# Kernel tuning notes

Hardware: AMD Instinct MI355X
Metric: run time of the kernel (lower is better)

Reference implementation:

```python
import jax, jax.numpy as jnp
import numpy as np

N_EMBED = 1024
HEAD_SIZE = 64
BLOCK_SIZE = 2048

def setup_inputs() -> dict:
    key = jax.random.key(0)
    kx, kq, kk, kv = jax.random.split(key, 4)
    scale = N_EMBED ** -0.5
    x = jax.random.normal(kx, (8, 2048, N_EMBED), dtype=jnp.float32)
    # nn.Linear weights stored as [out, in]; we keep [in, out] for x @ W
    Wq = jax.random.normal(kq, (N_EMBED, HEAD_SIZE), dtype=jnp.float32) * scale
    Wk = jax.random.normal(kk, (N_EMBED, HEAD_SIZE), dtype=jnp.float32) * scale
    Wv = jax.random.normal(kv, (N_EMBED, HEAD_SIZE), dtype=jnp.float32) * scale
    return {"x": x, "Wq": Wq, "Wk": Wk, "Wv": Wv}

def reference(x, Wq, Wk, Wv):
    B, T, C = x.shape
    q = x @ Wq  # [B,T,H]
    k = x @ Wk
    v = x @ Wv
    # NOTE: original scales by C**-0.5 (n_embed), not head_size**-0.5
    wei = jnp.einsum('bth,bsh->bts', q, k) * (C ** -0.5)  # [B,T,T]
    causal = jnp.tril(jnp.ones((T, T), dtype=bool))
    wei = jnp.where(causal, wei, -jnp.inf)
    wei = jax.nn.softmax(wei, axis=-1)
    out = jnp.einsum('bts,bsh->bth', wei, v)  # [B,T,H]
    return out
```

## Files before the change

kernel.cpp:

```cpp
#include <hip/hip_runtime.h>

#define B_ 8
#define T_ 2048
#define C_ 1024
#define H_ 64

typedef __attribute__((ext_vector_type(8))) short short8;
typedef __attribute__((ext_vector_type(4))) float floatx4;
typedef __attribute__((ext_vector_type(4))) int intx4;

static __device__ __forceinline__ unsigned short f2bf(float f) {
  unsigned int u = __builtin_bit_cast(unsigned int, f);
  u += 0x7FFFu + ((u >> 16) & 1u);
  return (unsigned short)(u >> 16);
}
static __device__ __forceinline__ unsigned short f2bf_t(float f) {
  return (unsigned short)(__builtin_bit_cast(unsigned int, f) >> 16);
}
static __device__ __forceinline__ float bf2f(unsigned short u) {
  return __builtin_bit_cast(float, ((unsigned int)u) << 16);
}
static __device__ __forceinline__ unsigned int fbits(float f) {
  return __builtin_bit_cast(unsigned int, f);
}

typedef const __attribute__((address_space(1))) unsigned int* gp1_t;
typedef __attribute__((address_space(3))) unsigned int* lp3_t;
static __device__ __forceinline__ void gl_lds16(const void* g, void* l) {
  __builtin_amdgcn_global_load_lds((gp1_t)g, (lp3_t)l, 16, 0, 0);
}

__global__ __launch_bounds__(256) void conv_w(const float* __restrict__ wq,
    const float* __restrict__ wk, const float* __restrict__ wv,
    unsigned short* __restrict__ wf) {
  int c = blockIdx.x * 256 + threadIdx.x;
  int lane = c & 63;
  int t = c >> 6;
  int ng = t % 12;
  int kk = t / 12;
  int k0 = kk * 32 + (lane >> 4) * 8;
  int n = ng * 16 + (lane & 15);
  const float* src;
  int col;
  float scale = 1.0f;
  if (n < 64)       { src = wq; col = n;       scale = 0.03125f * 1.44269504088896340736f; }
  else if (n < 128) { src = wk; col = n - 64;  }
  else              { src = wv; col = n - 128; }
  unsigned short o[8];
#pragma unroll
  for (int j = 0; j < 8; ++j) o[j] = f2bf(src[(size_t)(k0 + j) * H_ + col] * scale);
  *(uint4*)&wf[(size_t)c * 8] = *(const uint4*)o;
}

__global__ __launch_bounds__(256) void qkv_proj(
    const float* __restrict__ x, const unsigned short* __restrict__ wf,
    unsigned short* __restrict__ qo, unsigned short* __restrict__ kf,
    unsigned short* __restrict__ vf) {
  __shared__ float XL[2][2048];
  int tid = threadIdx.x;
  int wave = tid >> 6, lane = tid & 63;
  int lane4 = lane & 15, quad = lane >> 4;
  int m0 = blockIdx.x * 32;

  floatx4 acc[2][3];
#pragma unroll
  for (int mt = 0; mt < 2; ++mt)
#pragma unroll
    for (int nt = 0; nt < 3; ++nt) acc[mt][nt] = (floatx4)0.0f;

#pragma unroll
  for (int j = 0; j < 2; ++j) {
    int p = (wave * 2 + j) * 64 + lane;
    int r = p >> 4, pc = p & 15;
    int cl = (pc & 8) | ((pc ^ (r & 7)) & 7);
    gl_lds16(&x[(size_t)(m0 + r) * C_ + cl * 4], &XL[0][(wave * 2 + j) * 256]);
  }
  __syncthreads();

  for (int kt = 0; kt < 16; ++kt) {
    int buf = kt & 1;
    if (kt < 15) {
      int k0 = (kt + 1) * 64;
#pragma unroll
      for (int j = 0; j < 2; ++j) {
        int p = (wave * 2 + j) * 64 + lane;
        int r = p >> 4, pc = p & 15;
        int cl = (pc & 8) | ((pc ^ (r & 7)) & 7);
        gl_lds16(&x[(size_t)(m0 + r) * C_ + k0 + cl * 4], &XL[buf ^ 1][(wave * 2 + j) * 256]);
      }
    }

#pragma unroll
    for (int ks = 0; ks < 2; ++ks) {
      short8 b[3];
#pragma unroll
      for (int nt = 0; nt < 3; ++nt)
        b[nt] = *(const short8*)&wf[(size_t)(((kt * 2 + ks) * 12) + wave * 3 + nt) * 512 + lane * 8];
      short8 a[2];
#pragma unroll
      for (int mt = 0; mt < 2; ++mt) {
        int r = mt * 16 + lane4;
        int cl0 = ks * 8 + quad * 2;
        int pc0 = (cl0 & 8) | ((cl0 ^ (r & 7)) & 7);
        int pc1 = ((cl0 + 1) & 8) | (((cl0 + 1) ^ (r & 7)) & 7);
        float4 f0 = *(const float4*)&XL[buf][r * 64 + pc0 * 4];
        float4 f1 = *(const float4*)&XL[buf][r * 64 + pc1 * 4];
        intx4 pk;
        pk[0] = (int)__builtin_amdgcn_perm(fbits(f0.y), fbits(f0.x), 0x07060302u);
        pk[1] = (int)__builtin_amdgcn_perm(fbits(f0.w), fbits(f0.z), 0x07060302u);
        pk[2] = (int)__builtin_amdgcn_perm(fbits(f1.y), fbits(f1.x), 0x07060302u);
        pk[3] = (int)__builtin_amdgcn_perm(fbits(f1.w), fbits(f1.z), 0x07060302u);
        a[mt] = __builtin_bit_cast(short8, pk);
      }
#pragma unroll
      for (int mt = 0; mt < 2; ++mt)
#pragma unroll
        for (int nt = 0; nt < 3; ++nt)
          acc[mt][nt] = __builtin_amdgcn_mfma_f32_16x16x32_bf16(a[mt], b[nt], acc[mt][nt], 0, 0, 0);
    }
    __syncthreads();
  }

  unsigned short* VTB = (unsigned short*)&XL[0][0];
  unsigned short* KB  = VTB + 5120;
#pragma unroll
  for (int mt = 0; mt < 2; ++mt)
#pragma unroll
    for (int nt = 0; nt < 3; ++nt) {
      int n = wave * 48 + nt * 16 + lane4;
#pragma unroll
      for (int rr = 0; rr < 4; ++rr) {
        unsigned short val = f2bf(acc[mt][nt][rr]);
        int lrow = mt * 16 + quad * 4 + rr;
        if (n < 64)       qo[(size_t)(m0 + lrow) * H_ + n] = val;
        else if (n < 128) KB[lrow * 72 + (n - 64)] = val;
        else              VTB[(n - 128) * 40 + lrow] = val;
      }
    }
  __syncthreads();
  {
    int bb = m0 >> 11, t0 = m0 & 2047;
    int st = t0 >> 6, off = t0 & 63;
    int ks = tid >> 7, ctl = (tid >> 6) & 1, ln = tid & 63;
    int ct = (off >> 4) + ctl;
    int tl = ctl * 16 + (ln & 15);
    int h0 = ks * 32 + (ln >> 4) * 8;
    uint4 kd = *(const uint4*)&KB[tl * 72 + h0];
    *(uint4*)&kf[((size_t)((bb * 32 + st) * 2 + ks) * 4 + ct) * 512 + ln * 8] = kd;
    int nt = tid >> 6, l4 = tid & 15, qs = (tid >> 4) & 3;
    int ksv = off >> 5;
    uint4 vd = *(const uint4*)&VTB[(nt * 16 + l4) * 40 + qs * 8];
    *(uint4*)&vf[((size_t)((bb * 32 + st) * 2 + ksv) * 4 + nt) * 512 + (tid & 63) * 8] = vd;
  }
}

__global__ __launch_bounds__(256) void attn(
    const unsigned short* __restrict__ qi, const unsigned short* __restrict__ Kf,
    const unsigned short* __restrict__ Vf, unsigned short* __restrict__ Op,
    float* __restrict__ lsum) {
  __shared__ unsigned short PL[4][16][72];

  int tid = threadIdx.x;
  int wave = tid >> 6, lane = tid & 63;
  int lane4 = lane & 15, quad = lane >> 4;
  int qt = 31 - (int)blockIdx.x;
  int b = blockIdx.y, split = blockIdx.z;
  int qb = qt * 64;
  int base = b * T_;

  int ntile = qt + 1;
  int sBeg = (split * ntile) >> 2;
  int sEnd = ((split + 1) * ntile) >> 2;

  short8 aq[2];
#pragma unroll
  for (int ks = 0; ks < 2; ++ks)
    aq[ks] = *(const short8*)&qi[(size_t)(base + qb + wave * 16 + lane4) * H_ + ks * 32 + quad * 8];

  float lrow[4];
  floatx4 o[4];
#pragma unroll
  for (int r = 0; r < 4; ++r) lrow[r] = 0.0f;
#pragma unroll
  for (int nt = 0; nt < 4; ++nt) o[nt] = (floatx4)0.0f;

  for (int st = sBeg; st < sEnd; ++st) {
    size_t tb = (size_t)(b * 32 + st) * 8;
    short8 bk[2][4], bv[2][4];
#pragma unroll
    for (int ks = 0; ks < 2; ++ks)
#pragma unroll
      for (int ct = 0; ct < 4; ++ct)
        bk[ks][ct] = *(const short8*)&Kf[(tb + ks * 4 + ct) * 512 + lane * 8];
#pragma unroll
    for (int ks = 0; ks < 2; ++ks)
#pragma unroll
      for (int nt = 0; nt < 4; ++nt)
        bv[ks][nt] = *(const short8*)&Vf[(tb + ks * 4 + nt) * 512 + lane * 8];

    floatx4 sacc[4];
#pragma unroll
    for (int ct = 0; ct < 4; ++ct) sacc[ct] = (floatx4)0.0f;
#pragma unroll
    for (int ks = 0; ks < 2; ++ks)
#pragma unroll
      for (int ct = 0; ct < 4; ++ct)
        sacc[ct] = __builtin_amdgcn_mfma_f32_16x16x32_bf16(aq[ks], bk[ks][ct], sacc[ct], 0, 0, 0);

    if (st == qt) {
#pragma unroll
      for (int ct = 0; ct < 4; ++ct)
#pragma unroll
        for (int r = 0; r < 4; ++r) {
          int qrow = wave * 16 + quad * 4 + r;
          int scol = ct * 16 + lane4;
          if (scol > qrow) sacc[ct][r] = -3.0e38f;
        }
    }

#pragma unroll
    for (int ct = 0; ct < 4; ++ct)
#pragma unroll
      for (int r = 0; r < 4; ++r) {
        float p = exp2f(sacc[ct][r] - 8.0f);
        lrow[r] += p;
        PL[wave][quad * 4 + r][ct * 16 + lane4] = f2bf_t(p);
      }

#pragma unroll
    for (int ks = 0; ks < 2; ++ks) {
      short8 pa = *(const short8*)&PL[wave][lane4][ks * 32 + quad * 8];
#pragma unroll
      for (int nt = 0; nt < 4; ++nt)
        o[nt] = __builtin_amdgcn_mfma_f32_16x16x32_bf16(pa, bv[ks][nt], o[nt], 0, 0, 0);
    }
  }

#pragma unroll
  for (int off = 1; off < 16; off <<= 1)
#pragma unroll
    for (int r = 0; r < 4; ++r) lrow[r] += __shfl_xor(lrow[r], off);

  size_t pbase = (((size_t)split * 8 + b) * 32 + qt) * 64;
#pragma unroll
  for (int r = 0; r < 4; ++r) {
    int row = wave * 16 + quad * 4 + r;
#pragma unroll
    for (int nt = 0; nt < 4; ++nt)
      Op[(pbase + row) * 64 + nt * 16 + lane4] = f2bf(o[nt][r]);
    if (lane4 == 0) lsum[pbase + row] = lrow[r];
  }
}

__global__ __launch_bounds__(256) void merge_splits(
    const unsigned short* __restrict__ Op, const float* __restrict__ lsum,
    float* __restrict__ out) {
  int idx = blockIdx.x * 256 + threadIdx.x;
  int row = idx >> 4;
  int h4 = (idx & 15) * 4;
  int b = row >> 11, t = row & 2047;
  int qt = t >> 6, r = t & 63;
  float O0 = 0.f, O1 = 0.f, O2 = 0.f, O3 = 0.f, l = 0.f;
#pragma unroll
  for (int s = 0; s < 4; ++s) {
    size_t p = (((size_t)s * 8 + b) * 32 + qt) * 64 + r;
    l += lsum[p];
    ushort4 ov = *(const ushort4*)&Op[p * 64 + h4];
    O0 += bf2f(ov.x); O1 += bf2f(ov.y); O2 += bf2f(ov.z); O3 += bf2f(ov.w);
  }
  float inv = 1.0f / l;
  float4 res = make_float4(O0 * inv, O1 * inv, O2 * inv, O3 * inv);
  *(float4*)&out[(size_t)row * H_ + h4] = res;
}

extern "C" void kernel_launch(void* const* d_in, const int* in_sizes, int n_in,
                              void* d_out, int out_size, void* d_ws, size_t ws_size,
                              hipStream_t stream) {
  const float* x  = (const float*)d_in[0];
  const float* wq = (const float*)d_in[1];
  const float* wk = (const float*)d_in[2];
  const float* wv = (const float*)d_in[3];
  float* out = (float*)d_out;

  char* ws = (char*)d_ws;
  unsigned short* wf = (unsigned short*)ws;
  unsigned short* qb = (unsigned short*)(ws + 393216);
  unsigned short* kf = (unsigned short*)(ws + 2490368);
  unsigned short* vf = (unsigned short*)(ws + 4587520);
  unsigned short* Op = (unsigned short*)(ws + 6684672);
  float*          ls = (float*)(ws + 15073280);

  conv_w<<<96, 256, 0, stream>>>(wq, wk, wv, wf);
  qkv_proj<<<512, 256, 0, stream>>>(x, wf, qb, kf, vf);
  attn<<<dim3(32, 8, 4), 256, 0, stream>>>(qb, kf, vf, Op, ls);
  merge_splits<<<1024, 256, 0, stream>>>(Op, ls, out);
}
```

Baseline: 137.4 us.

## Halve QKV projection row tile and load whole x tile into LDS upfront

The projection kernel now handles 16 rows per block instead of 32 and launches 1024 blocks. The full 16x1024 fp32 slice of x (64KB) is loaded into LDS in one go, which replaces the double-buffered 64-column pipeline and removes the per-iteration barriers. The launch bounds request two blocks per CU. The aim is more parallelism and fewer syncs, at the cost of less reuse of the weight fragments (each B load now feeds one MFMA row tile instead of two) and no overlap between loading x and computing. The K/V scatter epilogue is rewritten for the 16-row tile.

Result: slower. 141.6 us (+3.1%).

```diff
diff --git a/kernel.cpp b/kernel.cpp
--- a/kernel.cpp
+++ b/kernel.cpp
@@ -52,105 +52,90 @@
   *(uint4*)&wf[(size_t)c * 8] = *(const uint4*)o;
 }
 
-__global__ __launch_bounds__(256) void qkv_proj(
+__global__ __launch_bounds__(256, 2) void qkv_proj(
     const float* __restrict__ x, const unsigned short* __restrict__ wf,
     unsigned short* __restrict__ qo, unsigned short* __restrict__ kf,
     unsigned short* __restrict__ vf) {
-  __shared__ float XL[2][2048];
+  __shared__ float XL[16384];
   int tid = threadIdx.x;
   int wave = tid >> 6, lane = tid & 63;
   int lane4 = lane & 15, quad = lane >> 4;
-  int m0 = blockIdx.x * 32;
-
-  floatx4 acc[2][3];
-#pragma unroll
-  for (int mt = 0; mt < 2; ++mt)
-#pragma unroll
-    for (int nt = 0; nt < 3; ++nt) acc[mt][nt] = (floatx4)0.0f;
-
-#pragma unroll
-  for (int j = 0; j < 2; ++j) {
-    int p = (wave * 2 + j) * 64 + lane;
-    int r = p >> 4, pc = p & 15;
-    int cl = (pc & 8) | ((pc ^ (r & 7)) & 7);
-    gl_lds16(&x[(size_t)(m0 + r) * C_ + cl * 4], &XL[0][(wave * 2 + j) * 256]);
+  int m0 = blockIdx.x * 16;
+
+#pragma unroll
+  for (int j = 0; j < 16; ++j) {
+    int p = (wave * 16 + j) * 64 + lane;
+    int r = p >> 8, pc = p & 255;
+    int cl = (pc & ~7) | ((pc ^ (r & 7)) & 7);
+    gl_lds16(&x[(size_t)(m0 + r) * C_ + cl * 4], &XL[(wave * 16 + j) * 256]);
   }
   __syncthreads();
 
+  floatx4 acc[3];
+#pragma unroll
+  for (int nt = 0; nt < 3; ++nt) acc[nt] = (floatx4)0.0f;
+
+#pragma unroll 4
   for (int kt = 0; kt < 16; ++kt) {
-    int buf = kt & 1;
-    if (kt < 15) {
-      int k0 = (kt + 1) * 64;
-#pragma unroll
-      for (int j = 0; j < 2; ++j) {
-        int p = (wave * 2 + j) * 64 + lane;
-        int r = p >> 4, pc = p & 15;
-        int cl = (pc & 8) | ((pc ^ (r & 7)) & 7);
-        gl_lds16(&x[(size_t)(m0 + r) * C_ + k0 + cl * 4], &XL[buf ^ 1][(wave * 2 + j) * 256]);
-      }
-    }
-
 #pragma unroll
     for (int ks = 0; ks < 2; ++ks) {
       short8 b[3];
 #pragma unroll
       for (int nt = 0; nt < 3; ++nt)
         b[nt] = *(const short8*)&wf[(size_t)(((kt * 2 + ks) * 12) + wave * 3 + nt) * 512 + lane * 8];
-      short8 a[2];
-#pragma unroll
-      for (int mt = 0; mt < 2; ++mt) {
-        int r = mt * 16 + lane4;
-        int cl0 = ks * 8 + quad * 2;
-        int pc0 = (cl0 & 8) | ((cl0 ^ (r & 7)) & 7);
-        int pc1 = ((cl0 + 1) & 8) | (((cl0 + 1) ^ (r & 7)) & 7);
-        float4 f0 = *(const float4*)&XL[buf][r * 64 + pc0 * 4];
-        float4 f1 = *(const float4*)&XL[buf][r * 64 + pc1 * 4];
-        intx4 pk;
-        pk[0] = (int)__builtin_amdgcn_perm(fbits(f0.y), fbits(f0.x), 0x07060302u);
-        pk[1] = (int)__builtin_amdgcn_perm(fbits(f0.w), fbits(f0.z), 0x07060302u);
-        pk[2] = (int)__builtin_amdgcn_perm(fbits(f1.y), fbits(f1.x), 0x07060302u);
-        pk[3] = (int)__builtin_amdgcn_perm(fbits(f1.w), fbits(f1.z), 0x07060302u);
-        a[mt] = __builtin_bit_cast(short8, pk);
-      }
-#pragma unroll
-      for (int mt = 0; mt < 2; ++mt)
-#pragma unroll
-        for (int nt = 0; nt < 3; ++nt)
-          acc[mt][nt] = __builtin_amdgcn_mfma_f32_16x16x32_bf16(a[mt], b[nt], acc[mt][nt], 0, 0, 0);
-    }
-    __syncthreads();
-  }
-
-  unsigned short* VTB = (unsigned short*)&XL[0][0];
-  unsigned short* KB  = VTB + 5120;
-#pragma unroll
-  for (int mt = 0; mt < 2; ++mt)
-#pragma unroll
-    for (int nt = 0; nt < 3; ++nt) {
-      int n = wave * 48 + nt * 16 + lane4;
-#pragma unroll
-      for (int rr = 0; rr < 4; ++rr) {
-        unsigned short val = f2bf(acc[mt][nt][rr]);
-        int lrow = mt * 16 + quad * 4 + rr;
-        if (n < 64)       qo[(size_t)(m0 + lrow) * H_ + n] = val;
-        else if (n < 128) KB[lrow * 72 + (n - 64)] = val;
-        else              VTB[(n - 128) * 40 + lrow] = val;
-      }
-    }
+      int r = lane4;
+      int c0 = kt * 16 + ks * 8 + quad * 2;
+      int pc0 = (c0 & ~7) | ((c0 ^ (r & 7)) & 7);
+      int pc1 = ((c0 + 1) & ~7) | (((c0 + 1) ^ (r & 7)) & 7);
+      float4 f0 = *(const float4*)&XL[r * 1024 + pc0 * 4];
+      float4 f1 = *(const float4*)&XL[r * 1024 + pc1 * 4];
+      intx4 pk;
+      pk[0] = (int)__builtin_amdgcn_perm(fbits(f0.y), fbits(f0.x), 0x07060302u);
+      pk[1] = (int)__builtin_amdgcn_perm(fbits(f0.w), fbits(f0.z), 0x07060302u);
+      pk[2] = (int)__builtin_amdgcn_perm(fbits(f1.y), fbits(f1.x), 0x07060302u);
+      pk[3] = (int)__builtin_amdgcn_perm(fbits(f1.w), fbits(f1.z), 0x07060302u);
+      short8 a = __builtin_bit_cast(short8, pk);
+#pragma unroll
+      for (int nt = 0; nt < 3; ++nt)
+        acc[nt] = __builtin_amdgcn_mfma_f32_16x16x32_bf16(a, b[nt], acc[nt], 0, 0, 0);
+    }
+  }
+
+  unsigned short* VTB = (unsigned short*)&XL[0];
+  unsigned short* KB  = VTB + 64 * 24;
+  __syncthreads();
+#pragma unroll
+  for (int nt = 0; nt < 3; ++nt) {
+    int n = wave * 48 + nt * 16 + lane4;
+#pragma unroll
+    for (int rr = 0; rr < 4; ++rr) {
+      unsigned short val = f2bf(acc[nt][rr]);
+      int lrow = quad * 4 + rr;
+      if (n < 64)       qo[(size_t)(m0 + lrow) * H_ + n] = val;
+      else if (n < 128) KB[lrow * 80 + (n - 64)] = val;
+      else              VTB[(n - 128) * 24 + lrow] = val;
+    }
+  }
   __syncthreads();
   {
     int bb = m0 >> 11, t0 = m0 & 2047;
-    int st = t0 >> 6, off = t0 & 63;
-    int ks = tid >> 7, ctl = (tid >> 6) & 1, ln = tid & 63;
-    int ct = (off >> 4) + ctl;
-    int tl = ctl * 16 + (ln & 15);
-    int h0 = ks * 32 + (ln >> 4) * 8;
-    uint4 kd = *(const uint4*)&KB[tl * 72 + h0];
-    *(uint4*)&kf[((size_t)((bb * 32 + st) * 2 + ks) * 4 + ct) * 512 + ln * 8] = kd;
-    int nt = tid >> 6, l4 = tid & 15, qs = (tid >> 4) & 3;
-    int ksv = off >> 5;
-    uint4 vd = *(const uint4*)&VTB[(nt * 16 + l4) * 40 + qs * 8];
-    *(uint4*)&vf[((size_t)((bb * 32 + st) * 2 + ksv) * 4 + nt) * 512 + (tid & 63) * 8] = vd;
+    int st = t0 >> 6;
+    if (tid < 128) {
+      int ks = tid >> 6, ln = tid & 63;
+      int ct = (t0 >> 4) & 3;
+      int tl = ln & 15;
+      int h0 = ks * 32 + (ln >> 4) * 8;
+      uint4 kd = *(const uint4*)&KB[tl * 80 + h0];
+      *(uint4*)&kf[((size_t)((bb * 32 + st) * 2 + ks) * 4 + ct) * 512 + ln * 8] = kd;
+    } else {
+      int u = tid - 128;
+      int nt = u >> 5, li = u & 31;
+      int ksv = (t0 >> 5) & 1;
+      int q0 = (t0 >> 3) & 3;
+      int qq = q0 + (li >> 4), l4 = li & 15;
+      uint4 vd = *(const uint4*)&VTB[(nt * 16 + l4) * 24 + (li >> 4) * 8];
+      *(uint4*)&vf[((size_t)((bb * 32 + st) * 2 + ksv) * 4 + nt) * 512 + (qq * 16 + l4) * 8] = vd;
+    }
   }
 }
 
@@ -291,7 +276,7 @@
   float*          ls = (float*)(ws + 15073280);
 
   conv_w<<<96, 256, 0, stream>>>(wq, wk, wv, wf);
-  qkv_proj<<<512, 256, 0, stream>>>(x, wf, qb, kf, vf);
+  qkv_proj<<<1024, 256, 0, stream>>>(x, wf, qb, kf, vf);
   attn<<<dim3(32, 8, 4), 256, 0, stream>>>(qb, kf, vf, Op, ls);
   merge_splits<<<1024, 256, 0, stream>>>(Op, ls, out);
 }
```

## Stage x in larger single-buffered 256-column phases in qkv_proj

Applied to the files above, without the earlier changes.

Replaces the double-buffered 64-column x staging loop (16 iterations, one barrier each) with four phases that each load a 256-column slab into one 32KB LDS buffer, synchronise, then run 8 MFMA k-slices. Launch bounds now request 4 blocks per CU so other blocks can hide load latency in place of in-block prefetch. This cuts barrier count and raises the bytes in flight per load, but loses overlap of loads with compute inside a block and raises LDS per block.

Result: faster. 132.7 us (-3.4%).

```diff
diff --git a/kernel.cpp b/kernel.cpp
--- a/kernel.cpp
+++ b/kernel.cpp
@@ -52,59 +52,57 @@
   *(uint4*)&wf[(size_t)c * 8] = *(const uint4*)o;
 }
 
-__global__ __launch_bounds__(256) void qkv_proj(
+__global__ __launch_bounds__(256, 4) void qkv_proj(
     const float* __restrict__ x, const unsigned short* __restrict__ wf,
     unsigned short* __restrict__ qo, unsigned short* __restrict__ kf,
     unsigned short* __restrict__ vf) {
-  __shared__ float XL[2][2048];
+  __shared__ float XL[8192];
   int tid = threadIdx.x;
   int wave = tid >> 6, lane = tid & 63;
   int lane4 = lane & 15, quad = lane >> 4;
   int m0 = blockIdx.x * 32;
 
+  auto stage_q = [&](int ph) {
+#pragma unroll
+    for (int j = 0; j < 8; ++j) {
+      int c = (wave * 8 + j) * 64 + lane;
+      int r = c >> 6, pc = c & 63;
+      int cl = (pc & ~7) | ((pc ^ (r & 7)) & 7);
+      gl_lds16(&x[(size_t)(m0 + r) * C_ + ph * 256 + cl * 4], &XL[c * 4]);
+    }
+  };
+
   floatx4 acc[2][3];
 #pragma unroll
   for (int mt = 0; mt < 2; ++mt)
 #pragma unroll
     for (int nt = 0; nt < 3; ++nt) acc[mt][nt] = (floatx4)0.0f;
 
-#pragma unroll
-  for (int j = 0; j < 2; ++j) {
-    int p = (wave * 2 + j) * 64 + lane;
-    int r = p >> 4, pc = p & 15;
-    int cl = (pc & 8) | ((pc ^ (r & 7)) & 7);
-    gl_lds16(&x[(size_t)(m0 + r) * C_ + cl * 4], &XL[0][(wave * 2 + j) * 256]);
-  }
+  stage_q(0);
   __syncthreads();
 
-  for (int kt = 0; kt < 16; ++kt) {
-    int buf = kt & 1;
-    if (kt < 15) {
-      int k0 = (kt + 1) * 64;
-#pragma unroll
-      for (int j = 0; j < 2; ++j) {
-        int p = (wave * 2 + j) * 64 + lane;
-        int r = p >> 4, pc = p & 15;
-        int cl = (pc & 8) | ((pc ^ (r & 7)) & 7);
-        gl_lds16(&x[(size_t)(m0 + r) * C_ + k0 + cl * 4], &XL[buf ^ 1][(wave * 2 + j) * 256]);
-      }
-    }
-
-#pragma unroll
-    for (int ks = 0; ks < 2; ++ks) {
+  for (int ph = 0; ph < 4; ++ph) {
+    if (ph) {
+      __syncthreads();
+      stage_q(ph);
+      __syncthreads();
+    }
+#pragma unroll
+    for (int sl = 0; sl < 8; ++sl) {
+      int s = ph * 8 + sl;
       short8 b[3];
 #pragma unroll
       for (int nt = 0; nt < 3; ++nt)
-        b[nt] = *(const short8*)&wf[(size_t)(((kt * 2 + ks) * 12) + wave * 3 + nt) * 512 + lane * 8];
+        b[nt] = *(const short8*)&wf[(size_t)(s * 12 + wave * 3 + nt) * 512 + lane * 8];
       short8 a[2];
 #pragma unroll
       for (int mt = 0; mt < 2; ++mt) {
         int r = mt * 16 + lane4;
-        int cl0 = ks * 8 + quad * 2;
-        int pc0 = (cl0 & 8) | ((cl0 ^ (r & 7)) & 7);
-        int pc1 = ((cl0 + 1) & 8) | (((cl0 + 1) ^ (r & 7)) & 7);
-        float4 f0 = *(const float4*)&XL[buf][r * 64 + pc0 * 4];
-        float4 f1 = *(const float4*)&XL[buf][r * 64 + pc1 * 4];
+        int c0 = sl * 8 + quad * 2;
+        int pc0 = (c0 & ~7) | ((c0 ^ (r & 7)) & 7);
+        int pc1 = ((c0 + 1) & ~7) | (((c0 + 1) ^ (r & 7)) & 7);
+        float4 f0 = *(const float4*)&XL[r * 256 + pc0 * 4];
+        float4 f1 = *(const float4*)&XL[r * 256 + pc1 * 4];
         intx4 pk;
         pk[0] = (int)__builtin_amdgcn_perm(fbits(f0.y), fbits(f0.x), 0x07060302u);
         pk[1] = (int)__builtin_amdgcn_perm(fbits(f0.w), fbits(f0.z), 0x07060302u);
@@ -118,11 +116,11 @@
         for (int nt = 0; nt < 3; ++nt)
           acc[mt][nt] = __builtin_amdgcn_mfma_f32_16x16x32_bf16(a[mt], b[nt], acc[mt][nt], 0, 0, 0);
     }
-    __syncthreads();
-  }
-
-  unsigned short* VTB = (unsigned short*)&XL[0][0];
+  }
+
+  unsigned short* VTB = (unsigned short*)&XL[0];
   unsigned short* KB  = VTB + 5120;
+  __syncthreads();
 #pragma unroll
   for (int mt = 0; mt < 2; ++mt)
 #pragma unroll
```
